# Kernel optimization log

Measured on AMD Instinct MI355X. Metric: run time of the kernel, lower is better.

## Reference

```python
import jax, jax.numpy as jnp
import numpy as np

NL = 2    # num_layers
H = 4     # attention heads
C = 512   # hidden_dim
IN = 256  # in_dim
F = 16    # fanout
B = 256   # seed nodes
NC = 47   # num_classes
DH = C // H
EPS = 1e-5


def _ln(x, g, b):
    mu = jnp.mean(x, -1, keepdims=True)
    var = jnp.mean((x - mu) ** 2, -1, keepdims=True)
    return (x - mu) * jax.lax.rsqrt(var + EPS) * g + b


def _mha(x, wqkv, bqkv, wo, bo):
    # torch nn.MultiheadAttention with a single batch of N tokens
    n = x.shape[0]
    qkv = x @ wqkv.T + bqkv                      # [N, 3C]
    q, k, v = jnp.split(qkv, 3, axis=-1)
    q = q.reshape(n, H, DH).transpose(1, 0, 2)   # [H, N, DH]
    k = k.reshape(n, H, DH).transpose(1, 0, 2)
    v = v.reshape(n, H, DH).transpose(1, 0, 2)
    s = jnp.einsum('hnd,hmd->hnm', q, k) * (1.0 / float(np.sqrt(DH)))
    a = jax.nn.softmax(s, axis=-1)
    o = jnp.einsum('hnm,hmd->hnd', a, v).transpose(1, 0, 2).reshape(n, C)
    return o @ wo.T + bo


def setup_inputs() -> dict:
    ks = jax.random.split(jax.random.key(0), 16)
    n = [B, B * F, B * F * F]
    p = lambda i, shape: jax.random.normal(ks[i], shape, jnp.float32) * 0.02
    return {
        'feats0': jax.random.normal(ks[0], (n[0], IN), jnp.float32),
        'feats1': jax.random.normal(ks[1], (n[1], IN), jnp.float32),
        'feats2': jax.random.normal(ks[2], (n[2], IN), jnp.float32),
        'nmask0': jnp.ones((n[0],), jnp.float32),
        'nmask1': jnp.ones((n[1],), jnp.float32),
        'nmask2': jnp.ones((n[2],), jnp.float32),
        'nbmask0': jax.random.randint(ks[3], (n[0], F), 0, 2, jnp.int32),
        'nbmask1': jax.random.randint(ks[4], (n[1], F), 0, 2, jnp.int32),
        'emb_w': p(5, (C, IN)), 'emb_b': jnp.zeros((C,), jnp.float32),
        'sage_w': p(6, (NL, C, 2 * C)), 'sage_b': jnp.zeros((NL, C), jnp.float32),
        'qkv_w': p(7, (NL, 3 * C, C)), 'qkv_b': jnp.zeros((NL, 3 * C), jnp.float32),
        'out_w': p(8, (NL, C, C)), 'out_b': jnp.zeros((NL, C), jnp.float32),
        'n1_g': jnp.ones((NL, C), jnp.float32), 'n1_b': jnp.zeros((NL, C), jnp.float32),
        'n2_g': jnp.ones((NL, C), jnp.float32), 'n2_b': jnp.zeros((NL, C), jnp.float32),
        'ffn_w1': p(9, (NL, 2 * C, C)), 'ffn_b1': jnp.zeros((NL, 2 * C), jnp.float32),
        'ffn_w2': p(10, (NL, C, 2 * C)), 'ffn_b2': jnp.zeros((NL, C), jnp.float32),
        'cls_w': p(11, (NC, C)), 'cls_b': jnp.zeros((NC,), jnp.float32),
    }


def reference(feats0, feats1, feats2, nmask0, nmask1, nmask2, nbmask0, nbmask1,
              emb_w, emb_b, sage_w, sage_b, qkv_w, qkv_b, out_w, out_b,
              n1_g, n1_b, n2_g, n2_b, ffn_w1, ffn_b1, ffn_w2, ffn_b2, cls_w, cls_b):
    nmasks = [nmask0, nmask1, nmask2]
    nbm = [nbmask0.astype(jnp.float32), nbmask1.astype(jnp.float32)]
    # embedding + node-mask gating per depth
    states = [(f @ emb_w.T + emb_b) * m[:, None]
              for f, m in zip([feats0, feats1, feats2], nmasks)]
    for li in range(NL):
        prev = states
        nxt = list(prev)
        for depth in range(NL - li - 1, -1, -1):
            # masked mean aggregation of sampled neighbors: [n_d, F, C] -> [n_d, C]
            child = prev[depth + 1].reshape(-1, F, C)
            m = nbm[depth][:, :, None]
            summed = jnp.sum(child * m, axis=1)
            denom = jnp.clip(jnp.sum(m, axis=1), 1.0)
            agg = summed / denom
            sf = prev[depth]
            # GraphSAGE concat update (no activation, dropout=0)
            h_local = jnp.concatenate([sf, agg], -1) @ sage_w[li].T + sage_b[li]
            h = _ln(sf + h_local, n1_g[li], n1_b[li])
            h = _ln(h + _mha(h, qkv_w[li], qkv_b[li], out_w[li], out_b[li]),
                    n2_g[li], n2_b[li])
            hf = jax.nn.relu(h @ ffn_w1[li].T + ffn_b1[li]) @ ffn_w2[li].T + ffn_b2[li]
            nxt[depth] = (h + hf) * nmasks[depth][:, None]
        states = nxt
    return states[0] @ cls_w.T + cls_b
```

## Files before the change

kernel.cpp:

```cpp
#include <hip/hip_runtime.h>
#include <math.h>


typedef unsigned short bf16_t;
typedef __attribute__((ext_vector_type(8))) short bf16x8_t;
typedef __attribute__((ext_vector_type(4))) float f32x4_t;

__device__ __forceinline__ bf16_t f2bf(float f) {
  union { float f; unsigned u; } v; v.f = f;
  unsigned r = v.u + 0x7FFFu + ((v.u >> 16) & 1u);
  return (bf16_t)(r >> 16);
}
__device__ __forceinline__ float bf2f(bf16_t u) {
  union { unsigned u; float f; } v; v.u = ((unsigned)u) << 16; return v.f;
}
__device__ __forceinline__ unsigned cvtpk(float lo, float hi) {
  unsigned r;
  asm("v_cvt_pk_bf16_f32 %0, %1, %2" : "=v"(r) : "v"(lo), "v"(hi));
  return r;
}
__device__ __forceinline__ void gload16(const void* g, void* l) {
  __builtin_amdgcn_global_load_lds(
      (const __attribute__((address_space(1))) unsigned int*)g,
      (__attribute__((address_space(3))) unsigned int*)l, 16, 0, 0);
}

#define QSCALE (0.08838834764831845f * 1.4426950408889634f)

template <int BM, int BN, int MODE, bool SPLIT>
__global__ __launch_bounds__(256) void mgemm(
    const bf16_t* __restrict__ A, const bf16_t* __restrict__ A2,
    const bf16_t* __restrict__ W, const float* __restrict__ bias,
    const bf16_t* __restrict__ res, const float* __restrict__ rowa,
    const float* __restrict__ rowb,
    bf16_t* __restrict__ Cb, bf16_t* __restrict__ Vt,
    int M, int N, int K) {
  constexpr int FM = BM / 32, FN = BN / 32;
  constexpr int NCH = (BM + BN) / 16;
  constexpr int CPW = NCH / 4;
  __shared__ bf16_t lds[2][(BM + BN) * 32];
  const int t = threadIdx.x;
  const int w = t >> 6, lane = t & 63;
  const int g = lane >> 4, li = lane & 15;
  const int bm = blockIdx.x * BM, bn = blockIdx.y * BN;
  const int wr = (w >> 1) * (BM / 2), wc = (w & 1) * (BN / 2);
  f32x4_t acc[FM][FN] = {};

  auto stage = [&](int buf, int k0) {
#pragma unroll
    for (int c0 = 0; c0 < CPW; ++c0) {
      const int c = w * CPW + c0;
      const int row = c * 16 + (lane >> 2);
      const int gk = k0 + (lane & 3) * 8;
      const bf16_t* src;
      if (row < BM) {
        if (SPLIT) {
          src = (gk < 512) ? (A + (size_t)(bm + row) * 512 + gk)
                           : (A2 + (size_t)(bm + row) * 512 + (gk - 512));
        } else {
          src = A + (size_t)(bm + row) * K + gk;
        }
      } else {
        src = W + (size_t)(bn + row - BM) * K + gk;
      }
      gload16(src, &lds[buf][c * 512]);
    }
  };

  const int nk = K / 32;
  stage(0, 0);
  for (int ks = 0; ks < nk; ++ks) {
    __syncthreads();
    if (ks + 1 < nk) stage((ks + 1) & 1, (ks + 1) * 32);
    const bf16_t* As = &lds[ks & 1][0];
    const bf16_t* Bs = &lds[ks & 1][BM * 32];
    bf16x8_t af[FM], bfr[FN];
#pragma unroll
    for (int i = 0; i < FM; ++i)
      af[i] = *(const bf16x8_t*)(As + (wr + i * 16 + li) * 32 + g * 8);
#pragma unroll
    for (int j = 0; j < FN; ++j)
      bfr[j] = *(const bf16x8_t*)(Bs + (wc + j * 16 + li) * 32 + g * 8);
#pragma unroll
    for (int i = 0; i < FM; ++i)
#pragma unroll
      for (int j = 0; j < FN; ++j)
        acc[i][j] = __builtin_amdgcn_mfma_f32_16x16x32_bf16(
            af[i], bfr[j], acc[i][j], 0, 0, 0);
  }

#pragma unroll
  for (int i = 0; i < FM; ++i) {
    const int mb = bm + wr + i * 16 + g * 4;
#pragma unroll
    for (int j = 0; j < FN; ++j) {
      const int n = bn + wc + j * 16 + li;
      if (MODE == 5) {
        const float bb = bias[n];
        if (n < 512) {
#pragma unroll
          for (int r = 0; r < 4; ++r)
            Cb[(size_t)(mb + r) * 1024 + n] = f2bf((acc[i][j][r] + bb) * QSCALE);
        } else if (n < 1024) {
#pragma unroll
          for (int r = 0; r < 4; ++r)
            Cb[(size_t)(mb + r) * 1024 + n] = f2bf(acc[i][j][r] + bb);
        } else {
          ushort4 o;
          o.x = f2bf(acc[i][j][0] + bb); o.y = f2bf(acc[i][j][1] + bb);
          o.z = f2bf(acc[i][j][2] + bb); o.w = f2bf(acc[i][j][3] + bb);
          *(ushort4*)(Vt + (size_t)(n - 1024) * M + mb) = o;
        }
      } else {
#pragma unroll
        for (int r = 0; r < 4; ++r) {
          const int m = mb + r;
          const float v = acc[i][j][r];
          if (MODE == 0) Cb[(size_t)m * N + n] = f2bf(v + bias[n]);
          if (MODE == 1) Cb[(size_t)m * N + n] = f2bf((v + bias[n]) * rowa[m]);
          if (MODE == 2)
            Cb[(size_t)m * N + n] = f2bf((v + bias[n] * rowa[m]) * rowb[m]);
          if (MODE == 3) Cb[(size_t)m * N + n] = f2bf(fmaxf(v + bias[n], 0.f));
          if (MODE == 4)
            Cb[(size_t)m * N + n] =
                f2bf((v + bias[n] + bf2f(res[(size_t)m * N + n])) * rowa[m]);
        }
      }
    }
  }
}

template <int QB, int SPLITS>
__global__ __launch_bounds__(QB * 4) void flashT(
    const bf16_t* __restrict__ qk, const bf16_t* __restrict__ vt,
    bf16_t* __restrict__ attno, bf16_t* __restrict__ Ofb,
    float* __restrict__ Ml, int N) {
  constexpr int NW = QB / 16;
  constexpr int KCH = 16 / NW;
  __shared__ bf16_t Ks[2][64 * 128];
  __shared__ bf16_t Vs[2][128 * 64];
  __shared__ bf16_t Ps[NW][16 * 64];
  const int bid = blockIdx.x;
  const int sp = bid % SPLITS;
  const int h = (bid / SPLITS) & 3;
  const int qb = bid / (4 * SPLITS);
  const int t = threadIdx.x, w = t >> 6, lane = t & 63;
  const int g = lane >> 4, li = lane & 15;
  const int kvbase = sp * (N / SPLITS);
  const int nt = (N / SPLITS) >> 6;

  bf16x8_t qf[4];
  {
    const bf16_t* qrow = qk + (size_t)(qb * QB + w * 16 + li) * 1024 + h * 128;
#pragma unroll
    for (int ks = 0; ks < 4; ++ks)
      qf[ks] = *(const bf16x8_t*)(qrow + ks * 32 + g * 8);
  }

  int koff[4], voff[2], pwoff[4];
#pragma unroll
  for (int ks = 0; ks < 4; ++ks)
    koff[ks] = li * 256 + (((ks * 4 + g) ^ (li & 7)) << 4);
#pragma unroll
  for (int ks = 0; ks < 2; ++ks)
    voff[ks] = li * 128 + (((ks * 4 + g) ^ (li & 7)) << 4);
#pragma unroll
  for (int mf = 0; mf < 4; ++mf)
    pwoff[mf] = li * 128 + (((mf * 2 + (g >> 1)) ^ (li & 7)) << 4) +
                ((g & 1) << 3);
  char* Pb = (char*)Ps + w * 2048;

  const bf16_t* kp[KCH];
  const bf16_t* vp[KCH];
#pragma unroll
  for (int i = 0; i < KCH; ++i) {
    const int c = w * KCH + i;
    const int rk = c * 4 + (lane >> 4);
    kp[i] = qk + (size_t)(kvbase + rk) * 1024 + 512 + h * 128 +
            (((lane & 15) ^ (rk & 7)) * 8);
    const int rv = c * 8 + (lane >> 3);
    vp[i] = vt + (size_t)(h * 128 + rv) * N + kvbase +
            (((lane & 7) ^ (rv & 7)) * 8);
  }
  auto stage = [&](int buf) {
#pragma unroll
    for (int i = 0; i < KCH; ++i) {
      const int c = w * KCH + i;
      gload16(kp[i], &Ks[buf][c * 512]);
      kp[i] += 64 * 1024;
      gload16(vp[i], &Vs[buf][c * 512]);
      vp[i] += 64;
    }
  };

  f32x4_t acc[8] = {};
  float mrun = -1e30f, lrun = 0.f;
  stage(0);
  for (int tt = 0; tt < nt; ++tt) {
    const int cur = tt & 1;
    __syncthreads();
    if (tt + 1 < nt) stage(cur ^ 1);
    const char* Kb = (const char*)Ks + cur * 16384;
    const char* Vb = (const char*)Vs + cur * 16384;

    f32x4_t sf[4] = {};
    __builtin_amdgcn_s_setprio(1);
#pragma unroll
    for (int ks = 0; ks < 4; ++ks) {
#pragma unroll
      for (int mf = 0; mf < 4; ++mf) {
        const bf16x8_t kf = *(const bf16x8_t*)(Kb + koff[ks] + mf * 4096);
        sf[mf] =
            __builtin_amdgcn_mfma_f32_16x16x32_bf16(kf, qf[ks], sf[mf], 0, 0, 0);
      }
    }
    __builtin_amdgcn_s_setprio(0);

    float tmax = -1e30f;
#pragma unroll
    for (int mf = 0; mf < 4; ++mf)
#pragma unroll
      for (int r = 0; r < 4; ++r) tmax = fmaxf(tmax, sf[mf][r]);
    tmax = fmaxf(tmax, __shfl_xor(tmax, 16));
    tmax = fmaxf(tmax, __shfl_xor(tmax, 32));
    if (!__all(tmax - mrun <= 11.0f)) {
      const float mnew = fmaxf(mrun, tmax);
      const float fsc = exp2f(mrun - mnew);
      mrun = mnew;
      lrun *= fsc;
#pragma unroll
      for (int mf = 0; mf < 8; ++mf) acc[mf] *= fsc;
    }
    float lsum = 0.f;
#pragma unroll
    for (int mf = 0; mf < 4; ++mf)
#pragma unroll
      for (int r = 0; r < 4; ++r) {
        const float p = exp2f(sf[mf][r] - mrun);
        sf[mf][r] = p;
        lsum += p;
      }
    lsum += __shfl_xor(lsum, 16);
    lsum += __shfl_xor(lsum, 32);
    lrun += lsum;

#pragma unroll
    for (int mf = 0; mf < 4; ++mf) {
      uint2 pv;
      pv.x = cvtpk(sf[mf][0], sf[mf][1]);
      pv.y = cvtpk(sf[mf][2], sf[mf][3]);
      *(uint2*)(Pb + pwoff[mf]) = pv;
    }
    __builtin_amdgcn_s_setprio(1);
#pragma unroll
    for (int ks = 0; ks < 2; ++ks) {
      const bf16x8_t pf = *(const bf16x8_t*)(Pb + voff[ks]);
#pragma unroll
      for (int mf = 0; mf < 8; ++mf) {
        const bf16x8_t vf = *(const bf16x8_t*)(Vb + voff[ks] + mf * 2048);
        acc[mf] =
            __builtin_amdgcn_mfma_f32_16x16x32_bf16(vf, pf, acc[mf], 0, 0, 0);
      }
    }
    __builtin_amdgcn_s_setprio(0);
  }

  const float invl = 1.f / lrun;
  const int q = qb * QB + w * 16 + li;
  if (SPLITS == 1) {
#pragma unroll
    for (int mf = 0; mf < 8; ++mf) {
      ushort4 o;
      o.x = f2bf(acc[mf][0] * invl); o.y = f2bf(acc[mf][1] * invl);
      o.z = f2bf(acc[mf][2] * invl); o.w = f2bf(acc[mf][3] * invl);
      *(ushort4*)(attno + (size_t)q * 512 + h * 128 + mf * 16 + g * 4) = o;
    }
  } else {
#pragma unroll
    for (int mf = 0; mf < 8; ++mf) {
      ushort4 o;
      o.x = f2bf(acc[mf][0] * invl); o.y = f2bf(acc[mf][1] * invl);
      o.z = f2bf(acc[mf][2] * invl); o.w = f2bf(acc[mf][3] * invl);
      *(ushort4*)(Ofb + ((size_t)sp * N + q) * 512 + h * 128 + mf * 16 +
                  g * 4) = o;
    }
    if (lane < 16) {
      float2 ml; ml.x = mrun; ml.y = lrun;
      *(float2*)(Ml + ((size_t)(sp * 4 + h) * N + q) * 2) = ml;
    }
  }
}

template <int SPLITS>
__global__ __launch_bounds__(256) void merge_attn(
    const bf16_t* __restrict__ Ofb, const float* __restrict__ Ml,
    bf16_t* __restrict__ attno, int N) {
  const int q = blockIdx.x, t = threadIdx.x;
#pragma unroll
  for (int half = 0; half < 2; ++half) {
    const int c = t + half * 256;
    const int h = c >> 7;
    float2 ml[SPLITS];
    float m = -1e30f;
#pragma unroll
    for (int s = 0; s < SPLITS; ++s) {
      ml[s] = ((const float2*)Ml)[(s * 4 + h) * N + q];
      m = fmaxf(m, ml[s].x);
    }
    float num = 0.f, den = 0.f;
#pragma unroll
    for (int s = 0; s < SPLITS; ++s) {
      const float wgt = ml[s].y * exp2f(ml[s].x - m);
      num += bf2f(Ofb[((size_t)s * N + q) * 512 + c]) * wgt;
      den += wgt;
    }
    attno[(size_t)q * 512 + c] = f2bf(num / den);
  }
}

__global__ __launch_bounds__(256) void add_ln(
    const bf16_t* __restrict__ X, const bf16_t* __restrict__ Y,
    const float* __restrict__ gg, const float* __restrict__ bb,
    bf16_t* __restrict__ out) {
  const int row = blockIdx.x, t = threadIdx.x;
  const size_t base = (size_t)row * 512;
  const float x0 = bf2f(X[base + t]) + bf2f(Y[base + t]);
  const float x1 = bf2f(X[base + 256 + t]) + bf2f(Y[base + 256 + t]);
  float s = x0 + x1, ss = x0 * x0 + x1 * x1;
#pragma unroll
  for (int o = 32; o > 0; o >>= 1) {
    s += __shfl_down(s, o);
    ss += __shfl_down(ss, o);
  }
  __shared__ float rs[4], rss[4], sm[2];
  const int wv = t >> 6, ln = t & 63;
  if (ln == 0) { rs[wv] = s; rss[wv] = ss; }
  __syncthreads();
  if (t == 0) {
    const float S = rs[0] + rs[1] + rs[2] + rs[3];
    const float SS = rss[0] + rss[1] + rss[2] + rss[3];
    const float mean = S * (1.f / 512.f);
    sm[0] = mean;
    sm[1] = rsqrtf(SS * (1.f / 512.f) - mean * mean + 1e-5f);
  }
  __syncthreads();
  const float mean = sm[0], rstd = sm[1];
  out[base + t] = f2bf((x0 - mean) * rstd * gg[t] + bb[t]);
  out[base + 256 + t] = f2bf((x1 - mean) * rstd * gg[t + 256] + bb[t + 256]);
}

__global__ __launch_bounds__(256) void agg_feats(
    const float* __restrict__ feats2, const int* __restrict__ nbm,
    const float* __restrict__ nm2, bf16_t* __restrict__ aggF,
    float* __restrict__ sw, float* __restrict__ invd) {
  const int i = blockIdx.x, t = threadIdx.x;
  float acc = 0.f, ws = 0.f, nbs = 0.f;
#pragma unroll
  for (int j = 0; j < 16; ++j) {
    const float nb = (float)nbm[i * 16 + j];
    const float wj = nb * nm2[i * 16 + j];
    acc += wj * feats2[(size_t)(i * 16 + j) * 256 + t];
    ws += wj;
    nbs += nb;
  }
  aggF[(size_t)i * 256 + t] = f2bf(acc);
  if (t == 0) { sw[i] = ws; invd[i] = 1.f / fmaxf(nbs, 1.f); }
}

__global__ __launch_bounds__(256) void agg_state(
    const bf16_t* __restrict__ src, const int* __restrict__ nbm,
    bf16_t* __restrict__ agg) {
  const int i = blockIdx.x, t = threadIdx.x;
  float a0 = 0.f, a1 = 0.f, nbs = 0.f;
#pragma unroll
  for (int j = 0; j < 16; ++j) {
    const float nb = (float)nbm[i * 16 + j];
    const bf16_t* r = src + (size_t)(i * 16 + j) * 512;
    a0 += nb * bf2f(r[t]);
    a1 += nb * bf2f(r[t + 256]);
    nbs += nb;
  }
  const float inv = 1.f / fmaxf(nbs, 1.f);
  agg[(size_t)i * 512 + t] = f2bf(a0 * inv);
  agg[(size_t)i * 512 + 256 + t] = f2bf(a1 * inv);
}

__global__ __launch_bounds__(256) void cvt_all(
    const float* __restrict__ s_emb, const float* __restrict__ s_sage,
    const float* __restrict__ s_qkv, const float* __restrict__ s_out,
    const float* __restrict__ s_f1, const float* __restrict__ s_f2,
    const float* __restrict__ s_ft0, const float* __restrict__ s_ft1,
    bf16_t* __restrict__ d_emb, bf16_t* __restrict__ d_sage,
    bf16_t* __restrict__ d_qkv, bf16_t* __restrict__ d_out,
    bf16_t* __restrict__ d_f1, bf16_t* __restrict__ d_f2,
    bf16_t* __restrict__ d_ft0, bf16_t* __restrict__ d_ft1) {
  int i = blockIdx.x * 256 + threadIdx.x;
  const float* s; bf16_t* d; int base;
  if (i < 32768)        { s = s_emb;  d = d_emb;  base = 0; }
  else if (i < 294912)  { s = s_sage; d = d_sage; base = 32768; }
  else if (i < 688128)  { s = s_qkv;  d = d_qkv;  base = 294912; }
  else if (i < 819200)  { s = s_out;  d = d_out;  base = 688128; }
  else if (i < 1081344) { s = s_f1;   d = d_f1;   base = 819200; }
  else if (i < 1343488) { s = s_f2;   d = d_f2;   base = 1081344; }
  else if (i < 1359872) { s = s_ft0;  d = d_ft0;  base = 1343488; }
  else                  { s = s_ft1;  d = d_ft1;  base = 1359872; }
  i -= base;
  const float4 v = ((const float4*)s)[i];
  ushort4 o;
  o.x = f2bf(v.x); o.y = f2bf(v.y); o.z = f2bf(v.z); o.w = f2bf(v.w);
  ((ushort4*)d)[i] = o;
}

__global__ __launch_bounds__(256) void cls_k(
    const bf16_t* __restrict__ s, const float* __restrict__ wc,
    const float* __restrict__ bc, float* __restrict__ out) {
  __shared__ float srow[512];
  const int m = blockIdx.x, t = threadIdx.x;
  srow[t] = bf2f(s[(size_t)m * 512 + t]);
  srow[t + 256] = bf2f(s[(size_t)m * 512 + 256 + t]);
  __syncthreads();
  if (t < 47) {
    float a = bc[t];
    const float* wr = wc + (size_t)t * 512;
    for (int k = 0; k < 512; ++k) a += srow[k] * wr[k];
    out[(size_t)m * 47 + t] = a;
  }
}

struct LayerW {
  const bf16_t *wsage, *wqkv, *wout, *wf1, *wf2;
  const float *bsage, *bqkv, *bout, *bf1, *bf2;
  const float *n1g, *n1b, *n2g, *n2b;
};
struct Scratch {
  bf16_t *tmpb, *h1, *h2, *qkb, *vt, *attno, *f1o, *Ofb;
  float *Ml;
};

static void run_block(int n, const bf16_t* sf, const bf16_t* agg,
                      const float* nmask, const LayerW& L, const Scratch& S,
                      bf16_t* sout, hipStream_t st) {
  if (n == 4096) {
    mgemm<64, 128, 0, true><<<dim3(64, 4), 256, 0, st>>>(
        sf, agg, L.wsage, L.bsage, nullptr, nullptr, nullptr, S.tmpb, nullptr,
        n, 512, 1024);
  } else {
    mgemm<64, 64, 0, true><<<dim3(4, 8), 256, 0, st>>>(
        sf, agg, L.wsage, L.bsage, nullptr, nullptr, nullptr, S.tmpb, nullptr,
        n, 512, 1024);
  }
  add_ln<<<n, 256, 0, st>>>(sf, S.tmpb, L.n1g, L.n1b, S.h1);
  if (n == 4096) {
    mgemm<128, 128, 5, false><<<dim3(32, 12), 256, 0, st>>>(
        S.h1, nullptr, L.wqkv, L.bqkv, nullptr, nullptr, nullptr,
        S.qkb, S.vt, n, 1536, 512);
    flashT<128, 4><<<(n / 128) * 16, 512, 0, st>>>(S.qkb, S.vt, nullptr, S.Ofb,
                                                   S.Ml, n);
    merge_attn<4><<<n, 256, 0, st>>>(S.Ofb, S.Ml, S.attno, n);
    mgemm<64, 128, 0, false><<<dim3(64, 4), 256, 0, st>>>(
        S.attno, nullptr, L.wout, L.bout, nullptr, nullptr, nullptr, S.tmpb,
        nullptr, n, 512, 512);
  } else {
    mgemm<64, 64, 5, false><<<dim3(4, 24), 256, 0, st>>>(
        S.h1, nullptr, L.wqkv, L.bqkv, nullptr, nullptr, nullptr,
        S.qkb, S.vt, n, 1536, 512);
    flashT<64, 1><<<(n / 64) * 4, 256, 0, st>>>(S.qkb, S.vt, S.attno, nullptr,
                                                nullptr, n);
    mgemm<64, 64, 0, false><<<dim3(4, 8), 256, 0, st>>>(
        S.attno, nullptr, L.wout, L.bout, nullptr, nullptr, nullptr, S.tmpb,
        nullptr, n, 512, 512);
  }
  add_ln<<<n, 256, 0, st>>>(S.h1, S.tmpb, L.n2g, L.n2b, S.h2);
  if (n == 4096) {
    mgemm<128, 128, 3, false><<<dim3(32, 8), 256, 0, st>>>(
        S.h2, nullptr, L.wf1, L.bf1, nullptr, nullptr, nullptr, S.f1o, nullptr,
        n, 1024, 512);
    mgemm<64, 128, 4, false><<<dim3(64, 4), 256, 0, st>>>(
        S.f1o, nullptr, L.wf2, L.bf2, S.h2, nmask, nullptr, sout, nullptr,
        n, 512, 1024);
  } else {
    mgemm<64, 64, 3, false><<<dim3(4, 16), 256, 0, st>>>(
        S.h2, nullptr, L.wf1, L.bf1, nullptr, nullptr, nullptr, S.f1o, nullptr,
        n, 1024, 512);
    mgemm<64, 64, 4, false><<<dim3(4, 8), 256, 0, st>>>(
        S.f1o, nullptr, L.wf2, L.bf2, S.h2, nmask, nullptr, sout, nullptr,
        n, 512, 1024);
  }
}

extern "C" void kernel_launch(void* const* d_in, const int* in_sizes, int n_in,
                              void* d_out, int out_size, void* d_ws,
                              size_t ws_size, hipStream_t stream) {
  const float* feats0 = (const float*)d_in[0];
  const float* feats1 = (const float*)d_in[1];
  const float* feats2 = (const float*)d_in[2];
  const float* nmask0 = (const float*)d_in[3];
  const float* nmask1 = (const float*)d_in[4];
  const float* nmask2 = (const float*)d_in[5];
  const int* nbmask0 = (const int*)d_in[6];
  const int* nbmask1 = (const int*)d_in[7];
  const float* emb_w = (const float*)d_in[8];
  const float* emb_b = (const float*)d_in[9];
  const float* sage_w = (const float*)d_in[10];
  const float* sage_b = (const float*)d_in[11];
  const float* qkv_w = (const float*)d_in[12];
  const float* qkv_b = (const float*)d_in[13];
  const float* out_w = (const float*)d_in[14];
  const float* out_b = (const float*)d_in[15];
  const float* n1_g = (const float*)d_in[16];
  const float* n1_b = (const float*)d_in[17];
  const float* n2_g = (const float*)d_in[18];
  const float* n2_b = (const float*)d_in[19];
  const float* ffn_w1 = (const float*)d_in[20];
  const float* ffn_b1 = (const float*)d_in[21];
  const float* ffn_w2 = (const float*)d_in[22];
  const float* ffn_b2 = (const float*)d_in[23];
  const float* cls_w = (const float*)d_in[24];
  const float* cls_b = (const float*)d_in[25];
  float* out = (float*)d_out;

  size_t off = 0;
  auto alloc = [&](size_t bytes) {
    void* r = (char*)d_ws + off;
    off += (bytes + 255) & ~(size_t)255;
    return r;
  };
  bf16_t* wemb = (bf16_t*)alloc((size_t)512 * 256 * 2);
  bf16_t* wsage = (bf16_t*)alloc((size_t)2 * 512 * 1024 * 2);
  bf16_t* wqkv = (bf16_t*)alloc((size_t)2 * 1536 * 512 * 2);
  bf16_t* wout = (bf16_t*)alloc((size_t)2 * 512 * 512 * 2);
  bf16_t* wf1 = (bf16_t*)alloc((size_t)2 * 1024 * 512 * 2);
  bf16_t* wf2 = (bf16_t*)alloc((size_t)2 * 512 * 1024 * 2);
  bf16_t* f0b = (bf16_t*)alloc((size_t)256 * 256 * 2);
  bf16_t* f1b = (bf16_t*)alloc((size_t)4096 * 256 * 2);
  bf16_t* s0 = (bf16_t*)alloc((size_t)256 * 512 * 2);
  bf16_t* s0b = (bf16_t*)alloc((size_t)256 * 512 * 2);
  bf16_t* s0f = (bf16_t*)alloc((size_t)256 * 512 * 2);
  bf16_t* s1 = (bf16_t*)alloc((size_t)4096 * 512 * 2);
  bf16_t* s1b = (bf16_t*)alloc((size_t)4096 * 512 * 2);
  bf16_t* aggFb = (bf16_t*)alloc((size_t)4096 * 256 * 2);
  float* swv = (float*)alloc((size_t)4096 * 4);
  float* invd = (float*)alloc((size_t)4096 * 4);
  bf16_t* aggb = (bf16_t*)alloc((size_t)4096 * 512 * 2);
  bf16_t* tmpb = (bf16_t*)alloc((size_t)4096 * 512 * 2);
  bf16_t* h1 = (bf16_t*)alloc((size_t)4096 * 512 * 2);
  bf16_t* h2 = (bf16_t*)alloc((size_t)4096 * 512 * 2);
  bf16_t* qkb = (bf16_t*)alloc((size_t)4096 * 1024 * 2);
  bf16_t* vt = (bf16_t*)alloc((size_t)512 * 4096 * 2);
  bf16_t* attno = (bf16_t*)alloc((size_t)4096 * 512 * 2);
  bf16_t* f1o = (bf16_t*)alloc((size_t)4096 * 1024 * 2);
  bf16_t* Ofb = (bf16_t*)alloc((size_t)4 * 4096 * 512 * 2);
  float* Ml = (float*)alloc((size_t)4 * 4 * 4096 * 2 * 4);

  cvt_all<<<6336, 256, 0, stream>>>(emb_w, sage_w, qkv_w, out_w, ffn_w1,
                                    ffn_w2, feats0, feats1, wemb, wsage, wqkv,
                                    wout, wf1, wf2, f0b, f1b);

  mgemm<64, 128, 1, false><<<dim3(64, 4), 256, 0, stream>>>(
      f1b, nullptr, wemb, emb_b, nullptr, nmask1, nullptr, s1, nullptr,
      4096, 512, 256);
  mgemm<64, 64, 1, false><<<dim3(4, 8), 256, 0, stream>>>(
      f0b, nullptr, wemb, emb_b, nullptr, nmask0, nullptr, s0, nullptr,
      256, 512, 256);
  agg_feats<<<4096, 256, 0, stream>>>(feats2, nbmask1, nmask2, aggFb, swv, invd);
  mgemm<64, 128, 2, false><<<dim3(64, 4), 256, 0, stream>>>(
      aggFb, nullptr, wemb, emb_b, nullptr, swv, invd, aggb, nullptr,
      4096, 512, 256);

  LayerW L0{wsage, wqkv, wout, wf1, wf2,
            sage_b, qkv_b, out_b, ffn_b1, ffn_b2,
            n1_g, n1_b, n2_g, n2_b};
  LayerW L1{wsage + 512 * 1024, wqkv + 1536 * 512, wout + 512 * 512,
            wf1 + 1024 * 512, wf2 + 512 * 1024,
            sage_b + 512, qkv_b + 1536, out_b + 512, ffn_b1 + 1024,
            ffn_b2 + 512, n1_g + 512, n1_b + 512, n2_g + 512, n2_b + 512};
  Scratch S{tmpb, h1, h2, qkb, vt, attno, f1o, Ofb, Ml};

  run_block(4096, s1, aggb, nmask1, L0, S, s1b, stream);
  agg_state<<<256, 256, 0, stream>>>(s1, nbmask0, aggb);
  run_block(256, s0, aggb, nmask0, L0, S, s0b, stream);
  agg_state<<<256, 256, 0, stream>>>(s1b, nbmask0, aggb);
  run_block(256, s0b, aggb, nmask0, L1, S, s0f, stream);

  cls_k<<<256, 256, 0, stream>>>(s0f, cls_w, cls_b, out);
}
```

Measured before the change: 311.4 us.

## Reuse K/V tiles across two query chunks per warp in flash attention; vectorize agg_feats

The flash attention kernel now lets each warp process several 16-row query chunks (NQC) against the same K and V tiles in shared memory. For n=4096 it runs 8 warps with 2 chunks each, giving 256-query blocks and half as many blocks, so K/V global loads and LDS staging are amortized over more queries. The cost is more accumulator registers per thread, which may lower occupancy. Separately, agg_feats now handles four nodes per block with float4 loads and stores instead of one scalar element per thread, and the host code is reorganized into two clean size branches.

```diff
diff --git a/kernel.cpp b/kernel.cpp
--- a/kernel.cpp
+++ b/kernel.cpp
@@ -130,12 +130,12 @@
   }
 }
 
-template <int QB, int SPLITS>
-__global__ __launch_bounds__(QB * 4) void flashT(
+template <int NW, int NQC, int SPLITS>
+__global__ __launch_bounds__(NW * 64) void flashT(
     const bf16_t* __restrict__ qk, const bf16_t* __restrict__ vt,
     bf16_t* __restrict__ attno, bf16_t* __restrict__ Ofb,
     float* __restrict__ Ml, int N) {
-  constexpr int NW = QB / 16;
+  constexpr int QB = NW * NQC * 16;
   constexpr int KCH = 16 / NW;
   __shared__ bf16_t Ks[2][64 * 128];
   __shared__ bf16_t Vs[2][128 * 64];
@@ -149,12 +149,14 @@
   const int kvbase = sp * (N / SPLITS);
   const int nt = (N / SPLITS) >> 6;
 
-  bf16x8_t qf[4];
-  {
-    const bf16_t* qrow = qk + (size_t)(qb * QB + w * 16 + li) * 1024 + h * 128;
+  bf16x8_t qf[NQC][4];
+#pragma unroll
+  for (int qc = 0; qc < NQC; ++qc) {
+    const bf16_t* qrow =
+        qk + (size_t)(qb * QB + w * (NQC * 16) + qc * 16 + li) * 1024 + h * 128;
 #pragma unroll
     for (int ks = 0; ks < 4; ++ks)
-      qf[ks] = *(const bf16x8_t*)(qrow + ks * 32 + g * 8);
+      qf[qc][ks] = *(const bf16x8_t*)(qrow + ks * 32 + g * 8);
   }
 
   int koff[4], voff[2], pwoff[4];
@@ -193,8 +195,11 @@
     }
   };
 
-  f32x4_t acc[8] = {};
-  float mrun = -1e30f, lrun = 0.f;
+  f32x4_t acc[NQC][8] = {};
+  float mrun[NQC], lrun[NQC];
+#pragma unroll
+  for (int qc = 0; qc < NQC; ++qc) { mrun[qc] = -1e30f; lrun[qc] = 0.f; }
+
   stage(0);
   for (int tt = 0; tt < nt; ++tt) {
     const int cur = tt & 1;
@@ -203,89 +208,107 @@
     const char* Kb = (const char*)Ks + cur * 16384;
     const char* Vb = (const char*)Vs + cur * 16384;
 
-    f32x4_t sf[4] = {};
+    f32x4_t sf[NQC][4];
+#pragma unroll
+    for (int qc = 0; qc < NQC; ++qc)
+#pragma unroll
+      for (int mf = 0; mf < 4; ++mf) sf[qc][mf] = (f32x4_t){0.f, 0.f, 0.f, 0.f};
     __builtin_amdgcn_s_setprio(1);
 #pragma unroll
     for (int ks = 0; ks < 4; ++ks) {
 #pragma unroll
       for (int mf = 0; mf < 4; ++mf) {
         const bf16x8_t kf = *(const bf16x8_t*)(Kb + koff[ks] + mf * 4096);
-        sf[mf] =
-            __builtin_amdgcn_mfma_f32_16x16x32_bf16(kf, qf[ks], sf[mf], 0, 0, 0);
+#pragma unroll
+        for (int qc = 0; qc < NQC; ++qc)
+          sf[qc][mf] = __builtin_amdgcn_mfma_f32_16x16x32_bf16(
+              kf, qf[qc][ks], sf[qc][mf], 0, 0, 0);
       }
     }
     __builtin_amdgcn_s_setprio(0);
 
-    float tmax = -1e30f;
-#pragma unroll
-    for (int mf = 0; mf < 4; ++mf)
-#pragma unroll
-      for (int r = 0; r < 4; ++r) tmax = fmaxf(tmax, sf[mf][r]);
-    tmax = fmaxf(tmax, __shfl_xor(tmax, 16));
-    tmax = fmaxf(tmax, __shfl_xor(tmax, 32));
-    if (!__all(tmax - mrun <= 11.0f)) {
-      const float mnew = fmaxf(mrun, tmax);
-      const float fsc = exp2f(mrun - mnew);
-      mrun = mnew;
-      lrun *= fsc;
-#pragma unroll
-      for (int mf = 0; mf < 8; ++mf) acc[mf] *= fsc;
-    }
-    float lsum = 0.f;
-#pragma unroll
-    for (int mf = 0; mf < 4; ++mf)
-#pragma unroll
-      for (int r = 0; r < 4; ++r) {
-        const float p = exp2f(sf[mf][r] - mrun);
-        sf[mf][r] = p;
-        lsum += p;
+    float tmax[NQC];
+#pragma unroll
+    for (int qc = 0; qc < NQC; ++qc) {
+      float tm = -1e30f;
+#pragma unroll
+      for (int mf = 0; mf < 4; ++mf)
+#pragma unroll
+        for (int r = 0; r < 4; ++r) tm = fmaxf(tm, sf[qc][mf][r]);
+      tm = fmaxf(tm, __shfl_xor(tm, 16));
+      tm = fmaxf(tm, __shfl_xor(tm, 32));
+      tmax[qc] = tm;
+    }
+    float worst = tmax[0] - mrun[0];
+#pragma unroll
+    for (int qc = 1; qc < NQC; ++qc)
+      worst = fmaxf(worst, tmax[qc] - mrun[qc]);
+    if (!__all(worst <= 11.0f)) {
+#pragma unroll
+      for (int qc = 0; qc < NQC; ++qc) {
+        const float mnew = fmaxf(mrun[qc], tmax[qc]);
+        const float fsc = exp2f(mrun[qc] - mnew);
+        mrun[qc] = mnew;
+        lrun[qc] *= fsc;
+#pragma unroll
+        for (int mf = 0; mf < 8; ++mf) acc[qc][mf] *= fsc;
       }
-    lsum += __shfl_xor(lsum, 16);
-    lsum += __shfl_xor(lsum, 32);
-    lrun += lsum;
-
-#pragma unroll
-    for (int mf = 0; mf < 4; ++mf) {
-      uint2 pv;
-      pv.x = cvtpk(sf[mf][0], sf[mf][1]);
-      pv.y = cvtpk(sf[mf][2], sf[mf][3]);
-      *(uint2*)(Pb + pwoff[mf]) = pv;
-    }
+    }
+#pragma unroll
+    for (int qc = 0; qc < NQC; ++qc) {
+      float lsum = 0.f;
+#pragma unroll
+      for (int mf = 0; mf < 4; ++mf)
+#pragma unroll
+        for (int r = 0; r < 4; ++r) {
+          const float p = exp2f(sf[qc][mf][r] - mrun[qc]);
+          sf[qc][mf][r] = p;
+          lsum += p;
+        }
+      lsum += __shfl_xor(lsum, 16);
+      lsum += __shfl_xor(lsum, 32);
+      lrun[qc] += lsum;
+    }
+
     __builtin_amdgcn_s_setprio(1);
 #pragma unroll
-    for (int ks = 0; ks < 2; ++ks) {
-      const bf16x8_t pf = *(const bf16x8_t*)(Pb + voff[ks]);
-#pragma unroll
-      for (int mf = 0; mf < 8; ++mf) {
-        const bf16x8_t vf = *(const bf16x8_t*)(Vb + voff[ks] + mf * 2048);
-        acc[mf] =
-            __builtin_amdgcn_mfma_f32_16x16x32_bf16(vf, pf, acc[mf], 0, 0, 0);
+    for (int qc = 0; qc < NQC; ++qc) {
+#pragma unroll
+      for (int mf = 0; mf < 4; ++mf) {
+        uint2 pv;
+        pv.x = cvtpk(sf[qc][mf][0], sf[qc][mf][1]);
+        pv.y = cvtpk(sf[qc][mf][2], sf[qc][mf][3]);
+        *(uint2*)(Pb + pwoff[mf]) = pv;
       }
+#pragma unroll
+      for (int ks = 0; ks < 2; ++ks) {
+        const bf16x8_t pf = *(const bf16x8_t*)(Pb + voff[ks]);
+#pragma unroll
+        for (int mf = 0; mf < 8; ++mf) {
+          const bf16x8_t vf = *(const bf16x8_t*)(Vb + voff[ks] + mf * 2048);
+          acc[qc][mf] = __builtin_amdgcn_mfma_f32_16x16x32_bf16(
+              vf, pf, acc[qc][mf], 0, 0, 0);
+        }
+      }
     }
     __builtin_amdgcn_s_setprio(0);
   }
 
-  const float invl = 1.f / lrun;
-  const int q = qb * QB + w * 16 + li;
-  if (SPLITS == 1) {
+#pragma unroll
+  for (int qc = 0; qc < NQC; ++qc) {
+    const float invl = 1.f / lrun[qc];
+    const int q = qb * QB + w * (NQC * 16) + qc * 16 + li;
+    bf16_t* dst = (SPLITS == 1) ? (attno + (size_t)q * 512 + h * 128)
+                                : (Ofb + ((size_t)sp * N + q) * 512 + h * 128);
 #pragma unroll
     for (int mf = 0; mf < 8; ++mf) {
       ushort4 o;
-      o.x = f2bf(acc[mf][0] * invl); o.y = f2bf(acc[mf][1] * invl);
-      o.z = f2bf(acc[mf][2] * invl); o.w = f2bf(acc[mf][3] * invl);
-      *(ushort4*)(attno + (size_t)q * 512 + h * 128 + mf * 16 + g * 4) = o;
-    }
-  } else {
-#pragma unroll
-    for (int mf = 0; mf < 8; ++mf) {
-      ushort4 o;
-      o.x = f2bf(acc[mf][0] * invl); o.y = f2bf(acc[mf][1] * invl);
-      o.z = f2bf(acc[mf][2] * invl); o.w = f2bf(acc[mf][3] * invl);
-      *(ushort4*)(Ofb + ((size_t)sp * N + q) * 512 + h * 128 + mf * 16 +
-                  g * 4) = o;
-    }
-    if (lane < 16) {
-      float2 ml; ml.x = mrun; ml.y = lrun;
+      o.x = f2bf(acc[qc][mf][0] * invl); o.y = f2bf(acc[qc][mf][1] * invl);
+      o.z = f2bf(acc[qc][mf][2] * invl); o.w = f2bf(acc[qc][mf][3] * invl);
+      *(ushort4*)(dst + mf * 16 + g * 4) = o;
+    }
+    if (SPLITS > 1 && lane < 16) {
+      float2 ml; ml.x = mrun[qc]; ml.y = lrun[qc];
       *(float2*)(Ml + ((size_t)(sp * 4 + h) * N + q) * 2) = ml;
     }
   }
@@ -353,18 +376,25 @@
     const float* __restrict__ feats2, const int* __restrict__ nbm,
     const float* __restrict__ nm2, bf16_t* __restrict__ aggF,
     float* __restrict__ sw, float* __restrict__ invd) {
-  const int i = blockIdx.x, t = threadIdx.x;
-  float acc = 0.f, ws = 0.f, nbs = 0.f;
+  const int node = blockIdx.x * 4 + (threadIdx.x >> 6);
+  const int lane = threadIdx.x & 63;
+  float4 acc = {0.f, 0.f, 0.f, 0.f};
+  float ws = 0.f, nbs = 0.f;
 #pragma unroll
   for (int j = 0; j < 16; ++j) {
-    const float nb = (float)nbm[i * 16 + j];
-    const float wj = nb * nm2[i * 16 + j];
-    acc += wj * feats2[(size_t)(i * 16 + j) * 256 + t];
+    const float nb = (float)nbm[node * 16 + j];
+    const float wj = nb * nm2[node * 16 + j];
+    const float4 v =
+        *(const float4*)(feats2 + (size_t)(node * 16 + j) * 256 + lane * 4);
+    acc.x += wj * v.x; acc.y += wj * v.y;
+    acc.z += wj * v.z; acc.w += wj * v.w;
     ws += wj;
     nbs += nb;
   }
-  aggF[(size_t)i * 256 + t] = f2bf(acc);
-  if (t == 0) { sw[i] = ws; invd[i] = 1.f / fmaxf(nbs, 1.f); }
+  ushort4 o;
+  o.x = f2bf(acc.x); o.y = f2bf(acc.y); o.z = f2bf(acc.z); o.w = f2bf(acc.w);
+  *(ushort4*)(aggF + (size_t)node * 256 + lane * 4) = o;
+  if (lane == 0) { sw[node] = ws; invd[node] = 1.f / fmaxf(nbs, 1.f); }
 }
 
 __global__ __launch_bounds__(256) void agg_state(
@@ -444,34 +474,17 @@
     mgemm<64, 128, 0, true><<<dim3(64, 4), 256, 0, st>>>(
         sf, agg, L.wsage, L.bsage, nullptr, nullptr, nullptr, S.tmpb, nullptr,
         n, 512, 1024);
-  } else {
-    mgemm<64, 64, 0, true><<<dim3(4, 8), 256, 0, st>>>(
-        sf, agg, L.wsage, L.bsage, nullptr, nullptr, nullptr, S.tmpb, nullptr,
-        n, 512, 1024);
-  }
-  add_ln<<<n, 256, 0, st>>>(sf, S.tmpb, L.n1g, L.n1b, S.h1);
-  if (n == 4096) {
+    add_ln<<<n, 256, 0, st>>>(sf, S.tmpb, L.n1g, L.n1b, S.h1);
     mgemm<128, 128, 5, false><<<dim3(32, 12), 256, 0, st>>>(
         S.h1, nullptr, L.wqkv, L.bqkv, nullptr, nullptr, nullptr,
         S.qkb, S.vt, n, 1536, 512);
-    flashT<128, 4><<<(n / 128) * 16, 512, 0, st>>>(S.qkb, S.vt, nullptr, S.Ofb,
-                                                   S.Ml, n);
+    flashT<8, 2, 4><<<(n / 256) * 16, 512, 0, st>>>(S.qkb, S.vt, nullptr,
+                                                    S.Ofb, S.Ml, n);
     merge_attn<4><<<n, 256, 0, st>>>(S.Ofb, S.Ml, S.attno, n);
     mgemm<64, 128, 0, false><<<dim3(64, 4), 256, 0, st>>>(
         S.attno, nullptr, L.wout, L.bout, nullptr, nullptr, nullptr, S.tmpb,
         nullptr, n, 512, 512);
-  } else {
-    mgemm<64, 64, 5, false><<<dim3(4, 24), 256, 0, st>>>(
-        S.h1, nullptr, L.wqkv, L.bqkv, nullptr, nullptr, nullptr,
-        S.qkb, S.vt, n, 1536, 512);
-    flashT<64, 1><<<(n / 64) * 4, 256, 0, st>>>(S.qkb, S.vt, S.attno, nullptr,
-                                                nullptr, n);
-    mgemm<64, 64, 0, false><<<dim3(4, 8), 256, 0, st>>>(
-        S.attno, nullptr, L.wout, L.bout, nullptr, nullptr, nullptr, S.tmpb,
-        nullptr, n, 512, 512);
-  }
-  add_ln<<<n, 256, 0, st>>>(S.h1, S.tmpb, L.n2g, L.n2b, S.h2);
-  if (n == 4096) {
+    add_ln<<<n, 256, 0, st>>>(S.h1, S.tmpb, L.n2g, L.n2b, S.h2);
     mgemm<128, 128, 3, false><<<dim3(32, 8), 256, 0, st>>>(
         S.h2, nullptr, L.wf1, L.bf1, nullptr, nullptr, nullptr, S.f1o, nullptr,
         n, 1024, 512);
@@ -479,6 +492,19 @@
         S.f1o, nullptr, L.wf2, L.bf2, S.h2, nmask, nullptr, sout, nullptr,
         n, 512, 1024);
   } else {
+    mgemm<64, 64, 0, true><<<dim3(4, 8), 256, 0, st>>>(
+        sf, agg, L.wsage, L.bsage, nullptr, nullptr, nullptr, S.tmpb, nullptr,
+        n, 512, 1024);
+    add_ln<<<n, 256, 0, st>>>(sf, S.tmpb, L.n1g, L.n1b, S.h1);
+    mgemm<64, 64, 5, false><<<dim3(4, 24), 256, 0, st>>>(
+        S.h1, nullptr, L.wqkv, L.bqkv, nullptr, nullptr, nullptr,
+        S.qkb, S.vt, n, 1536, 512);
+    flashT<4, 1, 1><<<(n / 64) * 4, 256, 0, st>>>(S.qkb, S.vt, S.attno,
+                                                  nullptr, nullptr, n);
+    mgemm<64, 64, 0, false><<<dim3(4, 8), 256, 0, st>>>(
+        S.attno, nullptr, L.wout, L.bout, nullptr, nullptr, nullptr, S.tmpb,
+        nullptr, n, 512, 512);
+    add_ln<<<n, 256, 0, st>>>(S.h1, S.tmpb, L.n2g, L.n2b, S.h2);
     mgemm<64, 64, 3, false><<<dim3(4, 16), 256, 0, st>>>(
         S.h2, nullptr, L.wf1, L.bf1, nullptr, nullptr, nullptr, S.f1o, nullptr,
         n, 1024, 512);
@@ -562,7 +588,7 @@
   mgemm<64, 64, 1, false><<<dim3(4, 8), 256, 0, stream>>>(
       f0b, nullptr, wemb, emb_b, nullptr, nmask0, nullptr, s0, nullptr,
       256, 512, 256);
-  agg_feats<<<4096, 256, 0, stream>>>(feats2, nbmask1, nmask2, aggFb, swv, invd);
+  agg_feats<<<1024, 256, 0, stream>>>(feats2, nbmask1, nmask2, aggFb, swv, invd);
   mgemm<64, 128, 2, false><<<dim3(64, 4), 256, 0, stream>>>(
       aggFb, nullptr, wemb, emb_b, nullptr, swv, invd, aggb, nullptr,
       4096, 512, 256);
```

After: 310.9 us. About the same (-0.1%).
